# Kernel optimization log

Measured on AMD Instinct MI355X. Metric: run time of the kernel, lower is better.

The kernel has to match this reference:

```python
import jax, jax.numpy as jnp
import numpy as np

IN_FEATURES = 1024
OUT_FEATURES = 1024
GRID_SIZE = 5
SPLINE_ORDER = 3
N_BASIS = GRID_SIZE + SPLINE_ORDER  # 8, matches spline_weight last dim
N_GRID = GRID_SIZE + 2 * SPLINE_ORDER + 1  # 12 knots -> Cox-de-Boor yields N_BASIS bases


def b_spline(x, grid):
    # x: [B, I] -> bases: [B, I, N_BASIS]
    x = x[..., None]
    bases = ((x >= grid[:-1]) & (x < grid[1:])).astype(x.dtype)
    for k in range(1, SPLINE_ORDER + 1):
        left = (x - grid[: -k - 1]) / (grid[k:-1] - grid[: -k - 1] + 1e-8)
        right = (grid[k + 1:] - x) / (grid[k + 1:] - grid[1:-k] + 1e-8)
        bases = left * bases[..., :-1] + right * bases[..., 1:]
    return bases


def setup_inputs() -> dict:
    key = jax.random.key(0)
    k1, k2, k3 = jax.random.split(key, 3)
    x = jax.random.uniform(k1, (4096, IN_FEATURES), dtype=jnp.float32) * 2.0 - 1.0
    # kaiming_uniform_(a=sqrt(5)) on [out,in]: bound = 1/sqrt(in)
    bound = 1.0 / np.sqrt(IN_FEATURES)
    base_weight = jax.random.uniform(k2, (OUT_FEATURES, IN_FEATURES), dtype=jnp.float32,
                                     minval=-bound, maxval=bound)
    spline_weight = 0.1 * jax.random.normal(k3, (OUT_FEATURES, IN_FEATURES, N_BASIS), dtype=jnp.float32)
    grid = jnp.linspace(-1.0, 1.0, N_GRID, dtype=jnp.float32)
    return {"x": x, "base_weight": base_weight, "spline_weight": spline_weight, "grid": grid}


def reference(x, base_weight, spline_weight, grid):
    base_output = jax.nn.silu(x) @ base_weight.T  # [B, O]
    spline_basis = b_spline(x, grid)              # [B, I, Q]
    spline_output = jnp.einsum('biq,oiq->bo', spline_basis, spline_weight)
    return base_output + spline_output
```

## Files before the change

kernel.cpp:

```cpp
#include <hip/hip_runtime.h>
#include <hip/hip_bf16.h>

#define IN_F 1024
#define OUT_F 1024
#define QP 9
#define KDIM (IN_F * QP)
#define BM 256
#define BN 256
#define BK 32

typedef __attribute__((ext_vector_type(8)))  short short8;
typedef __attribute__((ext_vector_type(16))) float floatx16;
typedef __attribute__((ext_vector_type(8)))  unsigned short ushort8v;

__device__ __forceinline__ unsigned short f2bf(float f) {
    union { float f; unsigned u; } v; v.f = f;
    return (unsigned short)((v.u + 0x7FFF + ((v.u >> 16) & 1)) >> 16);
}
__device__ __forceinline__ float bf2f(unsigned short h) {
    union { unsigned u; float f; } v; v.u = ((unsigned)h) << 16;
    return v.f;
}

__global__ __launch_bounds__(256) void pack_kernel(const float* __restrict__ x,
                                                   const float* __restrict__ bw,
                                                   const float* __restrict__ sw,
                                                   __hip_bfloat16* __restrict__ A,
                                                   __hip_bfloat16* __restrict__ W, int Bm) {
    const int nb_a = (Bm * IN_F / 8) / 256;
    if ((int)blockIdx.x < nb_a) {
        int t  = blockIdx.x * 256 + threadIdx.x;
        int b  = t >> 7;
        int i0 = (t & 127) * 8;
        const float4* xr = (const float4*)(x + (size_t)b * IN_F + i0);
        float4 x0 = xr[0], x1 = xr[1];
        float xv[8] = {x0.x, x0.y, x0.z, x0.w, x1.x, x1.y, x1.z, x1.w};
        ushort8v ov[9];
#pragma unroll
        for (int e = 0; e < 8; ++e) {
            float v  = xv[e];
            float u  = (v + 1.0f) * 5.5f;
            float fj = floorf(u);
            int   j  = (int)fj;
            float tt = u - fj;
            float t2 = tt * tt, t3 = t2 * tt;
            float omt = 1.0f - tt;
            float w0 = omt * omt * omt * (1.0f / 6.0f);
            float w1 = (3.0f * t3 - 6.0f * t2 + 4.0f) * (1.0f / 6.0f);
            float w2 = (-3.0f * t3 + 3.0f * t2 + 3.0f * tt + 1.0f) * (1.0f/6.0f);
            float w3 = t3 * (1.0f / 6.0f);
            ov[0][e] = f2bf(v * __builtin_amdgcn_rcpf(1.0f + __expf(-v)));
#pragma unroll
            for (int q = 0; q < 8; ++q) {
                int d = j - q;
                float bv = (d == 3) ? w0 : (d == 2) ? w1 : (d == 1) ? w2 : (d == 0) ? w3 : 0.0f;
                ov[1 + q][e] = f2bf(bv);
            }
        }
        unsigned short* dst = (unsigned short*)A + (size_t)b * KDIM + i0;
#pragma unroll
        for (int s = 0; s < QP; ++s)
            *(ushort8v*)(dst + (size_t)s * IN_F) = ov[s];
    } else {
        int t = ((int)blockIdx.x - nb_a) * 256 + threadIdx.x;
        unsigned short* dst = (unsigned short*)W + (size_t)(t >> 10) * KDIM + (t & 1023);
        dst[0] = f2bf(bw[t]);
        const float4* s4 = (const float4*)(sw + (size_t)t * 8);
        float4 lo = s4[0], hi = s4[1];
        dst[1 * IN_F] = f2bf(lo.x); dst[2 * IN_F] = f2bf(lo.y);
        dst[3 * IN_F] = f2bf(lo.z); dst[4 * IN_F] = f2bf(lo.w);
        dst[5 * IN_F] = f2bf(hi.x); dst[6 * IN_F] = f2bf(hi.y);
        dst[7 * IN_F] = f2bf(hi.z); dst[8 * IN_F] = f2bf(hi.w);
    }
}

#define GLD(src, dst) __builtin_amdgcn_global_load_lds( \
        (const __attribute__((address_space(1))) void*)(src), \
        (__attribute__((address_space(3))) void*)(dst), 16, 0, 0)

__global__ __launch_bounds__(512, 2) void gemm_splitk(const __hip_bfloat16* __restrict__ A,
                                                      const __hip_bfloat16* __restrict__ W,
                                                      unsigned short* __restrict__ P,
                                                      int Bm, int splitk, int kslice) {
    __shared__ short sA[3][BM * BK];
    __shared__ short sB[3][BN * BK];
    const int tid  = threadIdx.x;
    const int lane = tid & 63;
    const int wave = tid >> 6;
    const int r32  = lane & 31;
    const int half = lane >> 5;
    const int wm   = wave >> 2;
    const int wn   = wave & 3;

    const int b   = (int)blockIdx.x;
    const int xcd = b & 7, ii = b >> 3;
    const int pp  = xcd * (splitk >> 1) + (ii >> 4);
    const int xt  = pp & 3, zt = pp >> 2, yt = ii & 15;
    const int m0 = yt * BM, n0 = xt * BN, kb = zt * kslice;
    const int NT = kslice / BK;

    const short* Ag = (const short*)A + (size_t)m0 * KDIM + kb;
    const short* Wg = (const short*)W + (size_t)n0 * KDIM + kb;

    const int c0 = tid, c1 = 512 + tid;
    const int g0 = (c0 & 3) ^ ((c0 >> 3) & 3);
    const int g1 = (c1 & 3) ^ ((c1 >> 3) & 3);
    const short* pA0 = Ag + (size_t)(c0 >> 2) * KDIM + g0 * 8;
    const short* pA1 = Ag + (size_t)(c1 >> 2) * KDIM + g1 * 8;
    const short* pB0 = Wg + (size_t)(c0 >> 2) * KDIM + g0 * 8;
    const short* pB1 = Wg + (size_t)(c1 >> 2) * KDIM + g1 * 8;
    const int l0 = c0 * 8, l1 = c1 * 8;

    int offA[4][2], offB[2][2];
#pragma unroll
    for (int mi = 0; mi < 4; ++mi) {
        int row = wm * 128 + mi * 32 + r32;
        int sw  = (row >> 1) & 3;
#pragma unroll
        for (int kc = 0; kc < 2; ++kc)
            offA[mi][kc] = row * BK + (((kc * 2 + half) ^ sw) * 8);
    }
#pragma unroll
    for (int ni = 0; ni < 2; ++ni) {
        int row = wn * 64 + ni * 32 + r32;
        int sw  = (row >> 1) & 3;
#pragma unroll
        for (int kc = 0; kc < 2; ++kc)
            offB[ni][kc] = row * BK + (((kc * 2 + half) ^ sw) * 8);
    }

    floatx16 acc[4][2] = {};

#define STAGE(bi, koff) do { \
        GLD(pA0 + (koff), &sA[bi][l0]); \
        GLD(pA1 + (koff), &sA[bi][l1]); \
        GLD(pB0 + (koff), &sB[bi][l0]); \
        GLD(pB1 + (koff), &sB[bi][l1]); \
    } while (0)

    STAGE(0, 0);
    STAGE(1, BK);

    int bi = 0;
    for (int t = 0; t < NT; ++t) {
        if (t == NT - 1) asm volatile("s_waitcnt vmcnt(0) lgkmcnt(0)" ::: "memory");
        else             asm volatile("s_waitcnt vmcnt(4) lgkmcnt(0)" ::: "memory");
        __builtin_amdgcn_s_barrier();

        const short* sAb = &sA[bi][0];
        const short* sBb = &sB[bi][0];
        short8 aF[2][4], bF[2][2];
#pragma unroll
        for (int kc = 0; kc < 2; ++kc) {
#pragma unroll
            for (int mi = 0; mi < 4; ++mi) aF[kc][mi] = *(const short8*)(sAb + offA[mi][kc]);
#pragma unroll
            for (int ni = 0; ni < 2; ++ni) bF[kc][ni] = *(const short8*)(sBb + offB[ni][kc]);
        }

        if (t + 2 < NT) {
            int b2 = bi + 2; if (b2 >= 3) b2 -= 3;
            STAGE(b2, (t + 2) * BK);
        }

        __builtin_amdgcn_s_setprio(1);
#pragma unroll
        for (int kc = 0; kc < 2; ++kc)
#pragma unroll
            for (int mi = 0; mi < 4; ++mi)
#pragma unroll
                for (int ni = 0; ni < 2; ++ni)
                    acc[mi][ni] = __builtin_amdgcn_mfma_f32_32x32x16_bf16(
                        aF[kc][mi], bF[kc][ni], acc[mi][ni], 0, 0, 0);
        __builtin_amdgcn_s_setprio(0);

        if (++bi == 3) bi = 0;
    }
#undef STAGE

    unsigned short* Pz = P + (size_t)zt * Bm * OUT_F;
#pragma unroll
    for (int mi = 0; mi < 4; ++mi)
#pragma unroll
        for (int ni = 0; ni < 2; ++ni)
#pragma unroll
            for (int r = 0; r < 16; ++r) {
                int row = (r & 3) + 8 * (r >> 2) + 4 * half;
                int gm  = m0 + wm * 128 + mi * 32 + row;
                Pz[(size_t)gm * OUT_F + n0 + wn * 64 + ni * 32 + r32] = f2bf(acc[mi][ni][r]);
            }
}

__global__ __launch_bounds__(256) void reduce_kernel(const unsigned short* __restrict__ P,
                                                     float* __restrict__ C, int n, int s) {
    int t  = blockIdx.x * 256 + threadIdx.x;
    int i0 = t * 8;
    float o[8] = {0.f, 0.f, 0.f, 0.f, 0.f, 0.f, 0.f, 0.f};
    for (int j = 0; j < s; ++j) {
        ushort8v a = *(const ushort8v*)(P + (size_t)j * n + i0);
#pragma unroll
        for (int e = 0; e < 8; ++e) o[e] += bf2f(a[e]);
    }
    float4 o0, o1;
    o0.x = o[0]; o0.y = o[1]; o0.z = o[2]; o0.w = o[3];
    o1.x = o[4]; o1.y = o[5]; o1.z = o[6]; o1.w = o[7];
    *(float4*)(C + i0)     = o0;
    *(float4*)(C + i0 + 4) = o1;
}

__global__ __launch_bounds__(256) void fallback_kernel(const float* __restrict__ x,
                                                       const float* __restrict__ bw,
                                                       const float* __restrict__ sw,
                                                       const float* __restrict__ grid,
                                                       float* __restrict__ out, int Bm) {
    __shared__ float sv[256][QP + 1];
    int b = blockIdx.y;
    int o = blockIdx.x * 256 + threadIdx.x;
    float acc = 0.f;
    for (int ic = 0; ic < IN_F; ic += 256) {
        int i = ic + threadIdx.x;
        float v = x[(size_t)b * IN_F + i];
        float g[12];
        for (int j = 0; j < 12; ++j) g[j] = grid[j];
        float bb[11];
        for (int j = 0; j < 11; ++j) bb[j] = (v >= g[j] && v < g[j + 1]) ? 1.f : 0.f;
        for (int k = 1; k <= 3; ++k)
            for (int j = 0; j < 11 - k; ++j)
                bb[j] = (v - g[j]) / (g[j + k] - g[j] + 1e-8f) * bb[j]
                      + (g[j + k + 1] - v) / (g[j + k + 1] - g[j + 1] + 1e-8f) * bb[j + 1];
        __syncthreads();
        sv[threadIdx.x][0] = v / (1.f + __expf(-v));
        for (int q = 0; q < 8; ++q) sv[threadIdx.x][1 + q] = bb[q];
        __syncthreads();
        for (int ii = 0; ii < 256; ++ii) {
            int i2 = ic + ii;
            acc += sv[ii][0] * bw[(size_t)o * IN_F + i2];
            const float* swp = sw + ((size_t)o * IN_F + i2) * 8;
            for (int q = 0; q < 8; ++q) acc += sv[ii][1 + q] * swp[q];
        }
    }
    out[(size_t)b * OUT_F + o] = acc;
}

extern "C" void kernel_launch(void* const* d_in, const int* in_sizes, int n_in,
                              void* d_out, int out_size, void* d_ws, size_t ws_size,
                              hipStream_t stream) {
    const float* x    = (const float*)d_in[0];
    const float* bw   = (const float*)d_in[1];
    const float* sw   = (const float*)d_in[2];
    const float* grid = (const float*)d_in[3];
    float* out = (float*)d_out;

    const int Bm = in_sizes[0] / IN_F;
    const size_t a_bytes = (size_t)Bm * KDIM * sizeof(__hip_bfloat16);
    const size_t w_bytes = (size_t)OUT_F * KDIM * sizeof(__hip_bfloat16);

    int splitk = 4;
    size_t p_bytes = (size_t)splitk * Bm * OUT_F * sizeof(unsigned short);
    if (ws_size < a_bytes + w_bytes + p_bytes) {
        splitk = 2;
        p_bytes = (size_t)splitk * Bm * OUT_F * sizeof(unsigned short);
    }

    if (ws_size >= a_bytes + w_bytes + p_bytes && Bm == 4096) {
        __hip_bfloat16* Apk = (__hip_bfloat16*)d_ws;
        __hip_bfloat16* Wpk = (__hip_bfloat16*)((char*)d_ws + a_bytes);
        unsigned short* P = (unsigned short*)((char*)d_ws + a_bytes + w_bytes);
        const int nb_a = (Bm * IN_F / 8) / 256;
        const int nb_w = (OUT_F * IN_F) / 256;
        pack_kernel<<<nb_a + nb_w, 256, 0, stream>>>(x, bw, sw, Apk, Wpk, Bm);
        gemm_splitk<<<(Bm / BM) * (OUT_F / BN) * splitk, 512, 0, stream>>>(
            Apk, Wpk, P, Bm, splitk, KDIM / splitk);
        reduce_kernel<<<Bm * OUT_F / 2048, 256, 0, stream>>>(P, out, Bm * OUT_F, splitk);
    } else {
        fallback_kernel<<<dim3(OUT_F / 256, Bm), 256, 0, stream>>>(x, bw, sw, grid, out, Bm);
    }
}
```

Baseline: 200.0 us.

## Double K-tile depth to 64 and switch to double-buffered LDS pipeline

Raises the GEMM K tile from 32 to 64 and replaces the three-stage LDS ring with two buffers, reworking the XOR swizzle for 8 chunks per row. The aim is to halve barrier and wait overhead per unit of MFMA work. LDS fragment loads now sit inside the kc loop, which cuts register pressure. The trade-off is a prefetch distance of one tile with a full vmcnt(0) wait every iteration, plus one redundant tile load on the last iteration. It also assumes kslice is a multiple of 64.

Measured after the change: 197.5 us. No clear change (-1.3%).

```diff
diff --git a/kernel.cpp b/kernel.cpp
--- a/kernel.cpp
+++ b/kernel.cpp
@@ -7,7 +7,8 @@
 #define KDIM (IN_F * QP)
 #define BM 256
 #define BN 256
-#define BK 32
+#define BK 64
+#define TILE_SH (BM * BK)
 
 typedef __attribute__((ext_vector_type(8)))  short short8;
 typedef __attribute__((ext_vector_type(16))) float floatx16;
@@ -82,8 +83,8 @@
                                                       const __hip_bfloat16* __restrict__ W,
                                                       unsigned short* __restrict__ P,
                                                       int Bm, int splitk, int kslice) {
-    __shared__ short sA[3][BM * BK];
-    __shared__ short sB[3][BN * BK];
+    __shared__ __align__(16) short sA[2][TILE_SH];
+    __shared__ __align__(16) short sB[2][TILE_SH];
     const int tid  = threadIdx.x;
     const int lane = tid & 63;
     const int wave = tid >> 6;
@@ -102,81 +103,74 @@
     const short* Ag = (const short*)A + (size_t)m0 * KDIM + kb;
     const short* Wg = (const short*)W + (size_t)n0 * KDIM + kb;
 
-    const int c0 = tid, c1 = 512 + tid;
-    const int g0 = (c0 & 3) ^ ((c0 >> 3) & 3);
-    const int g1 = (c1 & 3) ^ ((c1 >> 3) & 3);
-    const short* pA0 = Ag + (size_t)(c0 >> 2) * KDIM + g0 * 8;
-    const short* pA1 = Ag + (size_t)(c1 >> 2) * KDIM + g1 * 8;
-    const short* pB0 = Wg + (size_t)(c0 >> 2) * KDIM + g0 * 8;
-    const short* pB1 = Wg + (size_t)(c1 >> 2) * KDIM + g1 * 8;
-    const int l0 = c0 * 8, l1 = c1 * 8;
-
-    int offA[4][2], offB[2][2];
+    const short* pA[4]; const short* pB[4]; int ldst[4];
+#pragma unroll
+    for (int u = 0; u < 4; ++u) {
+        int c  = u * 512 + tid;
+        int gs = ((c & 7) ^ ((c >> 3) & 7)) * 8;
+        pA[u] = Ag + (size_t)(c >> 3) * KDIM + gs;
+        pB[u] = Wg + (size_t)(c >> 3) * KDIM + gs;
+        ldst[u] = c * 8;
+    }
+
+    const int sw7 = r32 & 7;
+    int offA[4][4], offB[2][4];
 #pragma unroll
     for (int mi = 0; mi < 4; ++mi) {
         int row = wm * 128 + mi * 32 + r32;
-        int sw  = (row >> 1) & 3;
-#pragma unroll
-        for (int kc = 0; kc < 2; ++kc)
-            offA[mi][kc] = row * BK + (((kc * 2 + half) ^ sw) * 8);
+#pragma unroll
+        for (int kc = 0; kc < 4; ++kc)
+            offA[mi][kc] = row * BK + (((kc * 2 + half) ^ sw7) * 8);
     }
 #pragma unroll
     for (int ni = 0; ni < 2; ++ni) {
         int row = wn * 64 + ni * 32 + r32;
-        int sw  = (row >> 1) & 3;
-#pragma unroll
-        for (int kc = 0; kc < 2; ++kc)
-            offB[ni][kc] = row * BK + (((kc * 2 + half) ^ sw) * 8);
+#pragma unroll
+        for (int kc = 0; kc < 4; ++kc)
+            offB[ni][kc] = row * BK + (((kc * 2 + half) ^ sw7) * 8);
     }
 
     floatx16 acc[4][2] = {};
 
 #define STAGE(bi, koff) do { \
-        GLD(pA0 + (koff), &sA[bi][l0]); \
-        GLD(pA1 + (koff), &sA[bi][l1]); \
-        GLD(pB0 + (koff), &sB[bi][l0]); \
-        GLD(pB1 + (koff), &sB[bi][l1]); \
+        _Pragma("unroll") \
+        for (int u = 0; u < 4; ++u) { \
+            GLD(pA[u] + (koff), &sA[bi][ldst[u]]); \
+            GLD(pB[u] + (koff), &sB[bi][ldst[u]]); \
+        } \
     } while (0)
 
     STAGE(0, 0);
-    STAGE(1, BK);
-
-    int bi = 0;
+
     for (int t = 0; t < NT; ++t) {
-        if (t == NT - 1) asm volatile("s_waitcnt vmcnt(0) lgkmcnt(0)" ::: "memory");
-        else             asm volatile("s_waitcnt vmcnt(4) lgkmcnt(0)" ::: "memory");
+        asm volatile("s_waitcnt vmcnt(0)" ::: "memory");
         __builtin_amdgcn_s_barrier();
 
-        const short* sAb = &sA[bi][0];
-        const short* sBb = &sB[bi][0];
-        short8 aF[2][4], bF[2][2];
-#pragma unroll
-        for (int kc = 0; kc < 2; ++kc) {
-#pragma unroll
-            for (int mi = 0; mi < 4; ++mi) aF[kc][mi] = *(const short8*)(sAb + offA[mi][kc]);
-#pragma unroll
-            for (int ni = 0; ni < 2; ++ni) bF[kc][ni] = *(const short8*)(sBb + offB[ni][kc]);
-        }
-
-        if (t + 2 < NT) {
-            int b2 = bi + 2; if (b2 >= 3) b2 -= 3;
-            STAGE(b2, (t + 2) * BK);
-        }
+        const int nb = (t + 1 == NT) ? 0 : t + 1;
+        STAGE((t + 1) & 1, nb * BK);
+
+        const short* sAb = &sA[t & 1][0];
+        const short* sBb = &sB[t & 1][0];
 
         __builtin_amdgcn_s_setprio(1);
 #pragma unroll
-        for (int kc = 0; kc < 2; ++kc)
+        for (int kc = 0; kc < 4; ++kc) {
+            short8 aF[4], bF[2];
+#pragma unroll
+            for (int mi = 0; mi < 4; ++mi) aF[mi] = *(const short8*)(sAb + offA[mi][kc]);
+#pragma unroll
+            for (int ni = 0; ni < 2; ++ni) bF[ni] = *(const short8*)(sBb + offB[ni][kc]);
 #pragma unroll
             for (int mi = 0; mi < 4; ++mi)
 #pragma unroll
                 for (int ni = 0; ni < 2; ++ni)
                     acc[mi][ni] = __builtin_amdgcn_mfma_f32_32x32x16_bf16(
-                        aF[kc][mi], bF[kc][ni], acc[mi][ni], 0, 0, 0);
+                        aF[mi], bF[ni], acc[mi][ni], 0, 0, 0);
+        }
         __builtin_amdgcn_s_setprio(0);
-
-        if (++bi == 3) bi = 0;
     }
 #undef STAGE
+    asm volatile("s_waitcnt vmcnt(0)" ::: "memory");
 
     unsigned short* Pz = P + (size_t)zt * Bm * OUT_F;
 #pragma unroll
```
